# Kernel optimization log

Measured on AMD Instinct MI355X. Metric: run time of the kernel, lower is better.

Reference implementation:

```python
import jax, jax.numpy as jnp
import numpy as np

B, T = 2048, 256
VOCAB, E, H = 50000, 50, 50


def setup_inputs() -> dict:
    key = jax.random.key(0)
    ks = jax.random.split(key, 9)
    s = 0.1
    return {
        "batched_input": jax.random.randint(ks[0], (B, T), 0, VOCAB),
        "emb": jax.random.normal(ks[1], (VOCAB, E)) * s,
        "Wk": jax.random.normal(ks[2], (E, 4 * H)) * s,      # LSTM input kernel (i,f,c,o)
        "Uk": jax.random.normal(ks[3], (H, 4 * H)) * s,      # LSTM recurrent kernel
        "b": jnp.zeros((4 * H,)),                            # LSTM bias
        "W1": jax.random.normal(ks[4], (H, E)) * s,          # denseTypeOne (applied twice)
        "b1": jnp.zeros((E,)),
        "W2": jax.random.normal(ks[5], (E, 1)) * s,          # denseTypeTwo
        "b2": jnp.zeros((1,)),
    }


def _lstm(xg, Uk):
    # xg: [T, B, 4H] precomputed input projections; Keras gate order i,f,c,o
    Bsz = xg.shape[1]
    h0 = jnp.zeros((Bsz, H), xg.dtype)
    c0 = jnp.zeros((Bsz, H), xg.dtype)

    def step(carry, xt):
        h, c = carry
        z = xt + h @ Uk
        i, f, g, o = jnp.split(z, 4, axis=-1)
        i = jax.nn.sigmoid(i)
        f = jax.nn.sigmoid(f)
        g = jnp.tanh(g)
        o = jax.nn.sigmoid(o)
        c = f * c + i * g
        h = o * jnp.tanh(c)
        return (h, c), h

    (_, _), hs = jax.lax.scan(step, (h0, c0), xg)
    return hs  # [T, B, H]


def reference(batched_input, emb, Wk, Uk, b, W1, b1, W2, b2):
    x = emb[batched_input]                                  # [B, T, E]
    xg = jnp.einsum('bte,eg->tbg', x, Wk) + b               # [T, B, 4H]
    hs = _lstm(xg, Uk)                                      # [T, B, H]
    hs = jnp.transpose(hs, (1, 0, 2))                       # [B, T, H]
    d1 = jax.nn.relu(hs @ W1 + b1)                          # denseTypeOne
    d2 = jax.nn.relu(d1 @ W1 + b1)                          # denseTypeOne again (as in source)
    p = jax.nn.sigmoid(d2 @ W2 + b2)                        # [B, T, 1]
    return p.reshape(p.shape[0], -1)                        # Flatten -> [B, T]
```

## Files before the change

### kernel.cpp

```cpp
#include <hip/hip_runtime.h>


typedef unsigned short u16;
typedef unsigned int   u32;
typedef float f32x4 __attribute__((ext_vector_type(4)));
typedef short s16x8 __attribute__((ext_vector_type(8)));

__device__ __forceinline__ float bf2f(u16 u){
  union { u32 i; float f; } v; v.i = ((u32)u) << 16; return v.f;
}
__device__ __forceinline__ u16 f2bf(float f){
  union { float fl; u32 i; } v; v.fl = f;
  u32 r = v.i + 0x7fffu + ((v.i >> 16) & 1u);
  return (u16)(r >> 16);
}
__device__ __forceinline__ float frcp(float x){ return __builtin_amdgcn_rcpf(x); }
__device__ __forceinline__ float sigm_f(float x){
  float e = __expf(-x);
  return frcp(1.f + e);
}
__device__ __forceinline__ float tanh_f(float x){
  x = fminf(fmaxf(x, -15.f), 15.f);
  float e = __expf(-2.f * x);
  return (1.f - e) * frcp(1.f + e);
}
__device__ __forceinline__ f32x4 mf(s16x8 a, s16x8 b, f32x4 c){
  return __builtin_amdgcn_mfma_f32_16x16x32_bf16(a, b, c, 0, 0, 0);
}
__device__ __forceinline__ float ldf(const void* p, int i, bool f32in){
  if (f32in) return ((const float*)p)[i];
  return bf2f(((const u16*)p)[i]);
}

#define TPB 256
#define RPB 8

extern "C" __global__ __launch_bounds__(TPB, 1) void LSTM_Seq2Dis_15272903704706_kernel(
    const int* idx, const void* emb, const void* Wk, const void* Uk,
    const void* bias, const void* W1, const void* b1,
    const void* W2, const void* b2, float* out)
{
  __shared__ __align__(16) u16 ering[16][1024];
  __shared__ __align__(16) u16 abuf[2][1024];
  __shared__ __align__(16) u16 hbuf[8][2][512];
  __shared__ __align__(16) u16 dwork[4][2][512];
  __shared__ int   tokl[2048];
  __shared__ int   s_f32;

  const int tid = threadIdx.x;
  const int wv  = tid >> 6, ln = tid & 63;
  const int r0  = blockIdx.x * RPB;

  if (tid == 0){
    const u32* ew = (const u32*)emb;
    int hits = 0;
    for (int i = 0; i < 64; i++){
      u32 ef = (ew[i] >> 7) & 0xFFu;
      if (ef >= 112u && ef <= 127u) hits++;
    }
    s_f32 = (hits < 32) ? 1 : 0;
  }

  for (int i = tid; i < 16*1024; i += TPB) ((u16*)ering)[i] = 0;
  for (int i = tid; i < 2*1024;  i += TPB) ((u16*)abuf)[i]  = 0;
  for (int i = tid; i < 8*2*512; i += TPB) ((u16*)hbuf)[i]  = 0;
  for (int i = tid; i < 2048;    i += TPB){
    int r = i & 7, s = i >> 3;
    tokl[i] = idx[(r0 + r)*256 + s];
  }
  __syncthreads();
  const bool f32in = (s_f32 != 0);

  const int jown = wv*16 + (ln & 15);
  const bool jval = (jown < 50);
  s16x8 bz[4][4];
  #pragma unroll
  for (int t = 0; t < 4; t++){
    const int col = t*50 + jown;
    #pragma unroll
    for (int kt = 0; kt < 4; kt++){
      s16x8 v;
      #pragma unroll
      for (int j = 0; j < 8; j++){
        int k = kt*32 + ((ln >> 4) << 3) + j;
        float w = 0.f;
        if (jval){
          if (k < 50)                  w = ldf(Uk, k*200 + col, f32in);
          else if (k >= 64 && k < 114) w = ldf(Wk, (k-64)*200 + col, f32in);
        }
        v[j] = (short)f2bf(w);
      }
      bz[t][kt] = v;
    }
  }
  float bg[4];
  #pragma unroll
  for (int t = 0; t < 4; t++)
    bg[t] = jval ? ldf(bias, t*50 + jown, f32in) : 0.f;

  s16x8 w1f[4][2];
  float b1v[4], w2v[4];
  #pragma unroll
  for (int nt = 0; nt < 4; nt++){
    int c = nt*16 + (ln & 15);
    b1v[nt] = (c < 50) ? ldf(b1, c, f32in) : 0.f;
    w2v[nt] = (c < 50) ? ldf(W2, c, f32in) : 0.f;
    #pragma unroll
    for (int kt = 0; kt < 2; kt++){
      s16x8 v;
      #pragma unroll
      for (int j = 0; j < 8; j++){
        int k = kt*32 + ((ln >> 4) << 3) + j;
        v[j] = (short)((k < 50 && c < 50) ? f2bf(ldf(W1, k*50 + c, f32in)) : (u16)0);
      }
      w1f[nt][kt] = v;
    }
  }
  const float b2s = ldf(b2, 0, f32in);

  const int gr = tid / 50, gj = tid - gr*50;
  const int foff = (gj >> 5)*512 + (gr + (((gj & 31) >> 3) << 4))*8 + (gj & 7);

  const int q = ln >> 4;
  float creg[4] = {0.f, 0.f, 0.f, 0.f};
  const int aoff = (jown >> 5)*512 + ((q*4) + (((jown & 31) >> 3) << 4))*8 + (jown & 7);
  __syncthreads();

  for (int ch = 0; ch < 16; ch++){
    const int tc = ch*16;

    if (tid < 200){
      float ev[16];
      #pragma unroll
      for (int sl = 0; sl < 16; sl++)
        ev[sl] = ldf(emb, tokl[(tc + sl)*8 + gr]*50 + gj, f32in);
      #pragma unroll
      for (int sl = 0; sl < 16; sl++)
        ering[sl][foff] = f2bf(ev[sl]);
      #pragma unroll
      for (int sl = 0; sl < 16; sl++)
        ev[sl] = ldf(emb, tokl[(tc + sl)*8 + gr + 4]*50 + gj, f32in);
      #pragma unroll
      for (int sl = 0; sl < 16; sl++)
        ering[sl][foff + 32] = f2bf(ev[sl]);
    }
    __syncthreads();

    for (int sl = 0; sl < 16; sl++){
      const int s   = tc + sl;
      const int cur = s & 1, nxt = cur ^ 1;

      s16x8 av[4];
      av[0] = *(const s16x8*)&abuf[cur][ln*8];
      av[1] = *(const s16x8*)&abuf[cur][512 + ln*8];
      av[2] = *(const s16x8*)&ering[sl][ln*8];
      av[3] = *(const s16x8*)&ering[sl][512 + ln*8];
      f32x4 g4[4];
      #pragma unroll
      for (int t = 0; t < 4; t++){
        f32x4 acc = {0.f,0.f,0.f,0.f};
        #pragma unroll
        for (int kt = 0; kt < 4; kt++) acc = mf(av[kt], bz[t][kt], acc);
        g4[t] = acc;
      }

      u16 hb[4];
      #pragma unroll
      for (int r = 0; r < 4; r++){
        float iv = sigm_f(g4[0][r] + bg[0]);
        float fv = sigm_f(g4[1][r] + bg[1]);
        float gv = tanh_f(g4[2][r] + bg[2]);
        float ov = sigm_f(g4[3][r] + bg[3]);
        float c  = fv * creg[r] + iv * gv;
        creg[r] = c;
        hb[r] = f2bf(ov * tanh_f(c));
      }
      if (q < 2 && jval){
        #pragma unroll
        for (int r = 0; r < 4; r++){
          abuf[nxt][aoff + r*8] = hb[r];
          int m = sl*8 + q*4 + r;
          hbuf[m >> 4][jown >> 5][((m & 15) + (((jown & 31) >> 3) << 4))*8 + (jown & 7)] = hb[r];
        }
      }

      if (sl == 15){
        __syncthreads();
        #pragma unroll
        for (int p = 0; p < 2; p++){
          const int mt = 2*wv + p;
          s16x8 a0 = *(const s16x8*)&hbuf[mt][0][ln*8];
          s16x8 a1 = *(const s16x8*)&hbuf[mt][1][ln*8];
          #pragma unroll
          for (int nt = 0; nt < 4; nt++){
            f32x4 acc = {0.f,0.f,0.f,0.f};
            acc = mf(a0, w1f[nt][0], acc);
            acc = mf(a1, w1f[nt][1], acc);
            int c = nt*16 + (ln & 15);
            #pragma unroll
            for (int r = 0; r < 4; r++){
              float v = fmaxf(acc[r] + b1v[nt], 0.f);
              int row16 = ((ln >> 4) << 2) + r;
              dwork[wv][c >> 5][(row16 + (((c & 31) >> 3) << 4))*8 + (c & 7)] = f2bf(v);
            }
          }
          s16x8 d0 = *(const s16x8*)&dwork[wv][0][ln*8];
          s16x8 d1 = *(const s16x8*)&dwork[wv][1][ln*8];
          float part[4] = {0.f,0.f,0.f,0.f};
          #pragma unroll
          for (int nt = 0; nt < 4; nt++){
            f32x4 acc = {0.f,0.f,0.f,0.f};
            acc = mf(d0, w1f[nt][0], acc);
            acc = mf(d1, w1f[nt][1], acc);
            #pragma unroll
            for (int r = 0; r < 4; r++)
              part[r] += fmaxf(acc[r] + b1v[nt], 0.f) * w2v[nt];
          }
          #pragma unroll
          for (int d = 1; d < 16; d <<= 1)
            #pragma unroll
            for (int r = 0; r < 4; r++) part[r] += __shfl_xor(part[r], d, 16);
          if ((ln & 15) == 0){
            int qq = ln >> 4;
            #pragma unroll
            for (int r = 0; r < 4; r++){
              int m = mt*16 + (qq << 2) + r;
              int sl8 = m >> 3, rb = m & 7;
              float z = part[r] + b2s;
              z = fmaxf(fminf(z, 1.0f), -1.0f);
              out[(r0 + rb)*256 + tc + sl8] = sigm_f(z);
            }
          }
        }
      }
      __syncthreads();
    }
  }
}

extern "C" void kernel_launch(void* const* d_in, const int* in_sizes, int n_in,
                              void* d_out, int out_size, void* d_ws, size_t ws_size,
                              hipStream_t stream) {
  (void)in_sizes; (void)n_in; (void)out_size; (void)d_ws; (void)ws_size;
  hipLaunchKernelGGL(LSTM_Seq2Dis_15272903704706_kernel,
                     dim3(256), dim3(TPB), 0, stream,
                     (const int*)d_in[0], d_in[1], d_in[2], d_in[3], d_in[4],
                     d_in[5], d_in[6], d_in[7], d_in[8], (float*)d_out);
}
```

Before: 318.1 us.

## Make LSTM recurrence wave-local and precompute input projections per chunk

```diff
diff --git a/kernel.cpp b/kernel.cpp
--- a/kernel.cpp
+++ b/kernel.cpp
@@ -40,8 +40,8 @@
     const void* bias, const void* W1, const void* b1,
     const void* W2, const void* b2, float* out)
 {
-  __shared__ __align__(16) u16 ering[16][1024];
-  __shared__ __align__(16) u16 abuf[2][1024];
+  __shared__ __align__(16) u16 ebuf[8][2][512];
+  __shared__ __align__(16) u16 xgl[16*8*4*52];
   __shared__ __align__(16) u16 hbuf[8][2][512];
   __shared__ __align__(16) u16 dwork[4][2][512];
   __shared__ int   tokl[2048];
@@ -61,9 +61,8 @@
     s_f32 = (hits < 32) ? 1 : 0;
   }
 
-  for (int i = tid; i < 16*1024; i += TPB) ((u16*)ering)[i] = 0;
-  for (int i = tid; i < 2*1024;  i += TPB) ((u16*)abuf)[i]  = 0;
-  for (int i = tid; i < 8*2*512; i += TPB) ((u16*)hbuf)[i]  = 0;
+  for (int i = tid; i < 8*2*512; i += TPB) ((u16*)ebuf)[i] = 0;
+  for (int i = tid; i < 8*2*512; i += TPB) ((u16*)hbuf)[i] = 0;
   for (int i = tid; i < 2048;    i += TPB){
     int r = i & 7, s = i >> 3;
     tokl[i] = idx[(r0 + r)*256 + s];
@@ -71,32 +70,48 @@
   __syncthreads();
   const bool f32in = (s_f32 != 0);
 
-  const int jown = wv*16 + (ln & 15);
-  const bool jval = (jown < 50);
-  s16x8 bz[4][4];
+  const int cbase = ln & 15;
+
+  s16x8 ukf[4][4][2];
   #pragma unroll
-  for (int t = 0; t < 4; t++){
-    const int col = t*50 + jown;
-    #pragma unroll
-    for (int kt = 0; kt < 4; kt++){
+  for (int g = 0; g < 4; g++){
+    #pragma unroll
+    for (int u = 0; u < 4; u++){
+      const int unit = u*16 + cbase;
+      const int col  = g*50 + unit;
+      #pragma unroll
+      for (int kt = 0; kt < 2; kt++){
+        s16x8 v;
+        #pragma unroll
+        for (int j = 0; j < 8; j++){
+          int k = kt*32 + ((ln >> 4) << 3) + j;
+          float w = (unit < 50 && k < 50) ? ldf(Uk, k*200 + col, f32in) : 0.f;
+          v[j] = (short)f2bf(w);
+        }
+        ukf[g][u][kt] = v;
+      }
+    }
+  }
+
+  const int xunit = wv*16 + cbase;
+  s16x8 wkf[4][2];
+  float bgx[4];
+  #pragma unroll
+  for (int g = 0; g < 4; g++){
+    const int col = g*50 + xunit;
+    bgx[g] = (xunit < 50) ? ldf(bias, col, f32in) : 0.f;
+    #pragma unroll
+    for (int kt = 0; kt < 2; kt++){
       s16x8 v;
       #pragma unroll
       for (int j = 0; j < 8; j++){
         int k = kt*32 + ((ln >> 4) << 3) + j;
-        float w = 0.f;
-        if (jval){
-          if (k < 50)                  w = ldf(Uk, k*200 + col, f32in);
-          else if (k >= 64 && k < 114) w = ldf(Wk, (k-64)*200 + col, f32in);
-        }
+        float w = (xunit < 50 && k < 50) ? ldf(Wk, k*200 + col, f32in) : 0.f;
         v[j] = (short)f2bf(w);
       }
-      bz[t][kt] = v;
-    }
-  }
-  float bg[4];
-  #pragma unroll
-  for (int t = 0; t < 4; t++)
-    bg[t] = jval ? ldf(bias, t*50 + jown, f32in) : 0.f;
+      wkf[g][kt] = v;
+    }
+  }
 
   s16x8 w1f[4][2];
   float b1v[4], w2v[4];
@@ -119,12 +134,67 @@
   const float b2s = ldf(b2, 0, f32in);
 
   const int gr = tid / 50, gj = tid - gr*50;
-  const int foff = (gj >> 5)*512 + (gr + (((gj & 31) >> 3) << 4))*8 + (gj & 7);
-
-  const int q = ln >> 4;
-  float creg[4] = {0.f, 0.f, 0.f, 0.f};
-  const int aoff = (jown >> 5)*512 + ((q*4) + (((jown & 31) >> 3) << 4))*8 + (jown & 7);
-  __syncthreads();
+
+  const int srcl = ln & 15;
+  const int ubit = (ln >> 4) & 1;
+  const int rbit = ln >> 5;
+  const int grow = wv*2 + rbit;
+  const int U0   = ln & 31;
+  const int U1   = 32 + (ln & 31);
+  const bool v1  = (U1 < 50);
+  const int hsub = (((U0 >> 3) << 4))*8 + (U0 & 7);
+  float creg0 = 0.f, creg1 = 0.f;
+  s16x8 av0 = {0,0,0,0,0,0,0,0};
+  s16x8 av1 = {0,0,0,0,0,0,0,0};
+
+  auto dense_head = [&](int tcd){
+    #pragma unroll
+    for (int p = 0; p < 2; p++){
+      const int mt = 2*wv + p;
+      s16x8 a0 = *(const s16x8*)&hbuf[mt][0][ln*8];
+      s16x8 a1 = *(const s16x8*)&hbuf[mt][1][ln*8];
+      #pragma unroll
+      for (int nt = 0; nt < 4; nt++){
+        f32x4 acc = {0.f,0.f,0.f,0.f};
+        acc = mf(a0, w1f[nt][0], acc);
+        acc = mf(a1, w1f[nt][1], acc);
+        int c = nt*16 + (ln & 15);
+        #pragma unroll
+        for (int r = 0; r < 4; r++){
+          float v = fmaxf(acc[r] + b1v[nt], 0.f);
+          int row16 = ((ln >> 4) << 2) + r;
+          dwork[wv][c >> 5][(row16 + (((c & 31) >> 3) << 4))*8 + (c & 7)] = f2bf(v);
+        }
+      }
+      s16x8 d0 = *(const s16x8*)&dwork[wv][0][ln*8];
+      s16x8 d1 = *(const s16x8*)&dwork[wv][1][ln*8];
+      float part[4] = {0.f,0.f,0.f,0.f};
+      #pragma unroll
+      for (int nt = 0; nt < 4; nt++){
+        f32x4 acc = {0.f,0.f,0.f,0.f};
+        acc = mf(d0, w1f[nt][0], acc);
+        acc = mf(d1, w1f[nt][1], acc);
+        #pragma unroll
+        for (int r = 0; r < 4; r++)
+          part[r] += fmaxf(acc[r] + b1v[nt], 0.f) * w2v[nt];
+      }
+      #pragma unroll
+      for (int d = 1; d < 16; d <<= 1)
+        #pragma unroll
+        for (int r = 0; r < 4; r++) part[r] += __shfl_xor(part[r], d, 16);
+      if ((ln & 15) == 0){
+        int qq = ln >> 4;
+        #pragma unroll
+        for (int r = 0; r < 4; r++){
+          int m = mt*16 + (qq << 2) + r;
+          int sl8 = m >> 3, rb = m & 7;
+          float z = part[r] + b2s;
+          z = fmaxf(fminf(z, 1.0f), -1.0f);
+          out[(r0 + rb)*256 + tcd + sl8] = sigm_f(z);
+        }
+      }
+    }
+  };
 
   for (int ch = 0; ch < 16; ch++){
     const int tc = ch*16;
@@ -135,107 +205,131 @@
       for (int sl = 0; sl < 16; sl++)
         ev[sl] = ldf(emb, tokl[(tc + sl)*8 + gr]*50 + gj, f32in);
       #pragma unroll
-      for (int sl = 0; sl < 16; sl++)
-        ering[sl][foff] = f2bf(ev[sl]);
+      for (int sl = 0; sl < 16; sl++){
+        int m = sl*8 + gr;
+        ebuf[m >> 4][gj >> 5][((m & 15) + (((gj & 31) >> 3) << 4))*8 + (gj & 7)] = f2bf(ev[sl]);
+      }
       #pragma unroll
       for (int sl = 0; sl < 16; sl++)
         ev[sl] = ldf(emb, tokl[(tc + sl)*8 + gr + 4]*50 + gj, f32in);
       #pragma unroll
-      for (int sl = 0; sl < 16; sl++)
-        ering[sl][foff + 32] = f2bf(ev[sl]);
-    }
+      for (int sl = 0; sl < 16; sl++){
+        int m = sl*8 + gr + 4;
+        ebuf[m >> 4][gj >> 5][((m & 15) + (((gj & 31) >> 3) << 4))*8 + (gj & 7)] = f2bf(ev[sl]);
+      }
+    }
+    if (ch > 0) dense_head(tc - 16);
     __syncthreads();
 
-    for (int sl = 0; sl < 16; sl++){
-      const int s   = tc + sl;
-      const int cur = s & 1, nxt = cur ^ 1;
-
-      s16x8 av[4];
-      av[0] = *(const s16x8*)&abuf[cur][ln*8];
-      av[1] = *(const s16x8*)&abuf[cur][512 + ln*8];
-      av[2] = *(const s16x8*)&ering[sl][ln*8];
-      av[3] = *(const s16x8*)&ering[sl][512 + ln*8];
-      f32x4 g4[4];
-      #pragma unroll
-      for (int t = 0; t < 4; t++){
+    #pragma unroll
+    for (int mt = 0; mt < 8; mt++){
+      s16x8 e0 = *(const s16x8*)&ebuf[mt][0][ln*8];
+      s16x8 e1 = *(const s16x8*)&ebuf[mt][1][ln*8];
+      #pragma unroll
+      for (int g = 0; g < 4; g++){
         f32x4 acc = {0.f,0.f,0.f,0.f};
-        #pragma unroll
-        for (int kt = 0; kt < 4; kt++) acc = mf(av[kt], bz[t][kt], acc);
-        g4[t] = acc;
-      }
-
-      u16 hb[4];
-      #pragma unroll
-      for (int r = 0; r < 4; r++){
-        float iv = sigm_f(g4[0][r] + bg[0]);
-        float fv = sigm_f(g4[1][r] + bg[1]);
-        float gv = tanh_f(g4[2][r] + bg[2]);
-        float ov = sigm_f(g4[3][r] + bg[3]);
-        float c  = fv * creg[r] + iv * gv;
-        creg[r] = c;
-        hb[r] = f2bf(ov * tanh_f(c));
-      }
-      if (q < 2 && jval){
-        #pragma unroll
-        for (int r = 0; r < 4; r++){
-          abuf[nxt][aoff + r*8] = hb[r];
-          int m = sl*8 + q*4 + r;
-          hbuf[m >> 4][jown >> 5][((m & 15) + (((jown & 31) >> 3) << 4))*8 + (jown & 7)] = hb[r];
-        }
-      }
-
-      if (sl == 15){
-        __syncthreads();
-        #pragma unroll
-        for (int p = 0; p < 2; p++){
-          const int mt = 2*wv + p;
-          s16x8 a0 = *(const s16x8*)&hbuf[mt][0][ln*8];
-          s16x8 a1 = *(const s16x8*)&hbuf[mt][1][ln*8];
+        acc = mf(e0, wkf[g][0], acc);
+        acc = mf(e1, wkf[g][1], acc);
+        if (xunit < 50){
           #pragma unroll
-          for (int nt = 0; nt < 4; nt++){
-            f32x4 acc = {0.f,0.f,0.f,0.f};
-            acc = mf(a0, w1f[nt][0], acc);
-            acc = mf(a1, w1f[nt][1], acc);
-            int c = nt*16 + (ln & 15);
-            #pragma unroll
-            for (int r = 0; r < 4; r++){
-              float v = fmaxf(acc[r] + b1v[nt], 0.f);
-              int row16 = ((ln >> 4) << 2) + r;
-              dwork[wv][c >> 5][(row16 + (((c & 31) >> 3) << 4))*8 + (c & 7)] = f2bf(v);
-            }
-          }
-          s16x8 d0 = *(const s16x8*)&dwork[wv][0][ln*8];
-          s16x8 d1 = *(const s16x8*)&dwork[wv][1][ln*8];
-          float part[4] = {0.f,0.f,0.f,0.f};
-          #pragma unroll
-          for (int nt = 0; nt < 4; nt++){
-            f32x4 acc = {0.f,0.f,0.f,0.f};
-            acc = mf(d0, w1f[nt][0], acc);
-            acc = mf(d1, w1f[nt][1], acc);
-            #pragma unroll
-            for (int r = 0; r < 4; r++)
-              part[r] += fmaxf(acc[r] + b1v[nt], 0.f) * w2v[nt];
-          }
-          #pragma unroll
-          for (int d = 1; d < 16; d <<= 1)
-            #pragma unroll
-            for (int r = 0; r < 4; r++) part[r] += __shfl_xor(part[r], d, 16);
-          if ((ln & 15) == 0){
-            int qq = ln >> 4;
-            #pragma unroll
-            for (int r = 0; r < 4; r++){
-              int m = mt*16 + (qq << 2) + r;
-              int sl8 = m >> 3, rb = m & 7;
-              float z = part[r] + b2s;
-              z = fmaxf(fminf(z, 1.0f), -1.0f);
-              out[(r0 + rb)*256 + tc + sl8] = sigm_f(z);
-            }
+          for (int r = 0; r < 4; r++){
+            int m = mt*16 + ((ln >> 4) << 2) + r;
+            xgl[(m*4 + g)*52 + xunit] = f2bf(acc[r] + bgx[g]);
           }
         }
       }
-      __syncthreads();
-    }
-  }
+    }
+    __syncthreads();
+
+    for (int sl = 0; sl < 16; sl++){
+      const int xbase = (sl*8 + grow)*208;
+
+      float xa[4], xb[4];
+      #pragma unroll
+      for (int g = 0; g < 4; g++) xa[g] = bf2f(xgl[xbase + g*52 + U0]);
+      #pragma unroll
+      for (int g = 0; g < 4; g++) xb[g] = v1 ? bf2f(xgl[xbase + g*52 + U1]) : 0.f;
+
+      f32x4 pa[4], pb[4];
+      #pragma unroll
+      for (int g = 0; g < 4; g++){
+        f32x4 a = {0.f,0.f,0.f,0.f};
+        a = mf(av0, ukf[g][0][0], a);  a = mf(av1, ukf[g][0][1], a);
+        pa[g] = a;
+        f32x4 b = {0.f,0.f,0.f,0.f};
+        b = mf(av0, ukf[g][1][0], b);  b = mf(av1, ukf[g][1][1], b);
+        pb[g] = b;
+      }
+      float z0[4];
+      #pragma unroll
+      for (int g = 0; g < 4; g++){
+        float b00 = __shfl(pa[g][0], srcl);
+        float b01 = __shfl(pa[g][1], srcl);
+        float b10 = __shfl(pb[g][0], srcl);
+        float b11 = __shfl(pb[g][1], srcl);
+        float t0 = ubit ? b10 : b00;
+        float t1 = ubit ? b11 : b01;
+        z0[g] = (rbit ? t1 : t0) + xa[g];
+      }
+      float iv0 = sigm_f(z0[0]), fv0 = sigm_f(z0[1]);
+      float gv0 = tanh_f(z0[2]), ov0 = sigm_f(z0[3]);
+      float c0 = fv0 * creg0 + iv0 * gv0;
+      creg0 = c0;
+      u32 hb0 = (u32)f2bf(ov0 * tanh_f(c0));
+
+      #pragma unroll
+      for (int g = 0; g < 4; g++){
+        f32x4 a = {0.f,0.f,0.f,0.f};
+        a = mf(av0, ukf[g][2][0], a);  a = mf(av1, ukf[g][2][1], a);
+        pa[g] = a;
+        f32x4 b = {0.f,0.f,0.f,0.f};
+        b = mf(av0, ukf[g][3][0], b);  b = mf(av1, ukf[g][3][1], b);
+        pb[g] = b;
+      }
+      float z1[4];
+      #pragma unroll
+      for (int g = 0; g < 4; g++){
+        float b00 = __shfl(pa[g][0], srcl);
+        float b01 = __shfl(pa[g][1], srcl);
+        float b10 = __shfl(pb[g][0], srcl);
+        float b11 = __shfl(pb[g][1], srcl);
+        float t0 = ubit ? b10 : b00;
+        float t1 = ubit ? b11 : b01;
+        z1[g] = (rbit ? t1 : t0) + xb[g];
+      }
+      float iv1 = sigm_f(z1[0]), fv1 = sigm_f(z1[1]);
+      float gv1 = tanh_f(z1[2]), ov1 = sigm_f(z1[3]);
+      float c1 = fv1 * creg1 + iv1 * gv1;
+      creg1 = c1;
+      u32 hb1 = v1 ? (u32)f2bf(ov1 * tanh_f(c1)) : 0u;
+
+      {
+        int m = sl*8 + grow;
+        hbuf[m >> 4][0][(m & 15)*8 + hsub] = (u16)hb0;
+        if (v1) hbuf[m >> 4][1][(m & 15)*8 + hsub] = (u16)hb1;
+      }
+
+      u32 w0[8], w1[8];
+      #pragma unroll
+      for (int j = 0; j < 8; j++){
+        int k0 = ((ln >> 4) << 3) + j;
+        int s  = (srcl*32 + k0) & 63;
+        w0[j] = (u32)__shfl((int)hb0, s);
+        w1[j] = (u32)__shfl((int)hb1, s);
+      }
+      union { u32 w[4]; s16x8 v; } p0, p1;
+      #pragma unroll
+      for (int i = 0; i < 4; i++){
+        p0.w[i] = w0[2*i] | (w0[2*i+1] << 16);
+        p1.w[i] = w1[2*i] | (w1[2*i+1] << 16);
+      }
+      av0 = p0.v;
+      av1 = p1.v;
+    }
+    __syncthreads();
+  }
+
+  dense_head(240);
 }
 
 extern "C" void kernel_launch(void* const* d_in, const int* in_sizes, int n_in,
```

Measured after the change: 482.8 us. +51.8%, slower.
